# Kernel tuning notes

Measured on AMD Instinct MI355X. Metric: run time of the kernel, lower is better.

Reference implementation:

```python
import jax, jax.numpy as jnp
import numpy as np

N_EMBD = 1024
N_HEAD = 16
HEAD_DIM = N_EMBD // N_HEAD
SCALE = 1.0 / np.sqrt(HEAD_DIM).astype(np.float32)


def setup_inputs() -> dict:
    key = jax.random.key(0)
    ks = jax.random.split(key, 9)
    B, T = 2, 2048
    std = 1.0 / np.sqrt(N_EMBD).astype(np.float32)
    x = jax.random.normal(ks[0], (B, T, N_EMBD), dtype=jnp.float32)
    Wq = jax.random.normal(ks[1], (N_EMBD, N_EMBD), dtype=jnp.float32) * std
    Wk = jax.random.normal(ks[2], (N_EMBD, N_EMBD), dtype=jnp.float32) * std
    Wv = jax.random.normal(ks[3], (N_EMBD, N_EMBD), dtype=jnp.float32) * std
    Wo = jax.random.normal(ks[4], (N_EMBD, N_EMBD), dtype=jnp.float32) * std
    bq = jax.random.normal(ks[5], (N_EMBD,), dtype=jnp.float32) * 0.01
    bk = jax.random.normal(ks[6], (N_EMBD,), dtype=jnp.float32) * 0.01
    bv = jax.random.normal(ks[7], (N_EMBD,), dtype=jnp.float32) * 0.01
    bo = jax.random.normal(ks[8], (N_EMBD,), dtype=jnp.float32) * 0.01
    return {"x": x, "Wq": Wq, "bq": bq, "Wk": Wk, "bk": bk,
            "Wv": Wv, "bv": bv, "Wo": Wo, "bo": bo}


def reference(x, Wq, bq, Wk, bk, Wv, bv, Wo, bo):
    B, T, C = x.shape
    # project and split heads: (B, H, T, D)
    def heads(y):
        return y.reshape(B, T, N_HEAD, HEAD_DIM).transpose(0, 2, 1, 3)
    q = heads(x @ Wq.T + bq)
    k = heads(x @ Wk.T + bk)
    v = heads(x @ Wv.T + bv)
    # materialized causal attention (matches the torch module's math)
    att = jnp.einsum("bhqd,bhkd->bhqk", q, k) * SCALE
    causal = jnp.tril(jnp.ones((T, T), dtype=bool))
    att = jnp.where(causal, att, -jnp.inf)
    att = jax.nn.softmax(att, axis=-1)
    out = jnp.einsum("bhqk,bhkd->bhqd", att, v)
    out = out.transpose(0, 2, 1, 3).reshape(B, T, C)
    return out @ Wo.T + bo
```

## Files before the change

kernel.cpp:

```cpp
#include <hip/hip_runtime.h>
#include <stdint.h>

typedef unsigned short u16;
typedef __attribute__((ext_vector_type(8))) short short8;
typedef __attribute__((ext_vector_type(4))) float f32x4;
typedef __attribute__((ext_vector_type(16))) float f32x16;

__device__ __forceinline__ u16 f2bf(float f) {
  union { float f; unsigned int u; } c; c.f = f;
  return (u16)((c.u + 0x7FFFu + ((c.u >> 16) & 1u)) >> 16);
}

__device__ __forceinline__ float bf2f(u16 v) {
  union { unsigned int u; float f; } c; c.u = ((unsigned int)v) << 16;
  return c.f;
}

__device__ __forceinline__ f32x4 mfma16(short8 a, short8 b, f32x4 c) {
  return __builtin_amdgcn_mfma_f32_16x16x32_bf16(a, b, c, 0, 0, 0);
}

__device__ __forceinline__ f32x16 mfma32(short8 a, short8 b, f32x16 c) {
  return __builtin_amdgcn_mfma_f32_32x32x16_bf16(a, b, c, 0, 0, 0);
}

__device__ __forceinline__ void gl_lds16(const u16* g, u16* l) {
  __builtin_amdgcn_global_load_lds((const __attribute__((address_space(1))) void*)g,
                                   (__attribute__((address_space(3))) void*)l, 16, 0, 0);
}

__global__ __launch_bounds__(256) void cast_all(
    const float* __restrict__ x, const float* __restrict__ wq, const float* __restrict__ wk,
    const float* __restrict__ wv, const float* __restrict__ wo,
    u16* __restrict__ xb, u16* __restrict__ wqb, u16* __restrict__ wkb,
    u16* __restrict__ wvb, u16* __restrict__ wob) {
  int b = blockIdx.x;
  const float* src; u16* dst; int i;
  if (b < 4096)      { src = x;  dst = xb;  i = b * 256 + threadIdx.x; }
  else if (b < 5120) { src = wq; dst = wqb; i = (b - 4096) * 256 + threadIdx.x; }
  else if (b < 6144) { src = wk; dst = wkb; i = (b - 5120) * 256 + threadIdx.x; }
  else if (b < 7168) { src = wv; dst = wvb; i = (b - 6144) * 256 + threadIdx.x; }
  else               { src = wo; dst = wob; i = (b - 7168) * 256 + threadIdx.x; }
  float4 v = ((const float4*)src)[i];
  ushort4 o;
  o.x = f2bf(v.x); o.y = f2bf(v.y); o.z = f2bf(v.z); o.w = f2bf(v.w);
  ((ushort4*)dst)[i] = o;
}

__global__ __launch_bounds__(256) void qkv_gemm(
    const u16* __restrict__ xb, const u16* __restrict__ wqb, const u16* __restrict__ wkb,
    const u16* __restrict__ wvb, const float* __restrict__ bq, const float* __restrict__ bk,
    const float* __restrict__ bv, u16* __restrict__ Qb, u16* __restrict__ Kb,
    u16* __restrict__ VTb) {
  __shared__ __align__(16) u16 As[128 * 64];
  __shared__ __align__(16) u16 Bs[128 * 64];
  const int id = blockIdx.x;
  const int s = id >> 3;
  const int mblk = (id & 7) + ((s & 3) << 3);
  const int z = (s >> 2) % 3;
  const int nblk = s / 12;
  const u16* __restrict__ W = (z == 0) ? wqb : (z == 1) ? wkb : wvb;
  const float* __restrict__ bias = (z == 0) ? bq : (z == 1) ? bk : bv;
  const int m0 = mblk * 128, n0 = nblk * 128;
  const int tid = threadIdx.x, lane = tid & 63, wave = tid >> 6;
  const int wr = (wave >> 1) * 64, wc = (wave & 1) * 64;
  const int fr = lane & 15, fg = lane >> 4;
  const int lrow = lane >> 3;
  const int lcol = (((lane & 7) ^ (lrow & 7)) * 8);

  const u16* ga = xb + (size_t)(m0 + wave * 32 + lrow) * 1024 + lcol;
  const u16* gb = W  + (size_t)(n0 + wave * 32 + lrow) * 1024 + lcol;
  u16* la = As + wave * 2048;
  u16* lb = Bs + wave * 2048;

  f32x4 acc[4][4] = {};

  for (int k0 = 0; k0 < 1024; k0 += 64) {
#pragma unroll
    for (int i = 0; i < 4; ++i) {
      gl_lds16(ga + k0 + (size_t)(8 * i) * 1024, la + i * 512);
      gl_lds16(gb + k0 + (size_t)(8 * i) * 1024, lb + i * 512);
    }
    __syncthreads();
#pragma unroll
    for (int kk = 0; kk < 2; ++kk) {
      short8 a[4], b[4];
#pragma unroll
      for (int i = 0; i < 4; ++i)
        a[i] = *(const short8*)(As + (wr + i * 16 + fr) * 64 +
                                (((kk * 4 + fg) ^ (fr & 7)) * 8));
#pragma unroll
      for (int i = 0; i < 4; ++i)
        b[i] = *(const short8*)(Bs + (wc + i * 16 + fr) * 64 +
                                (((kk * 4 + fg) ^ (fr & 7)) * 8));
#pragma unroll
      for (int i = 0; i < 4; ++i)
#pragma unroll
        for (int j = 0; j < 4; ++j) acc[i][j] = mfma16(a[i], b[j], acc[i][j]);
    }
    __syncthreads();
  }

  const float qsc = (z == 0) ? (0.125f * 1.44269504088896f) : 1.0f;
#pragma unroll
  for (int j = 0; j < 4; ++j) {
    const int col = n0 + wc + j * 16 + fr;
    const float bcol = bias[col];
    const int h = col >> 6, d = col & 63;
#pragma unroll
    for (int i = 0; i < 4; ++i) {
#pragma unroll
      for (int r = 0; r < 4; ++r) {
        const int m = m0 + wr + i * 16 + fg * 4 + r;
        const int bi = m >> 11, t = m & 2047;
        const u16 o = f2bf((acc[i][j][r] + bcol) * qsc);
        const size_t bse = (size_t)(bi * 16 + h) << 17;
        if (z == 0)      Qb[bse + (size_t)t * 64 + d] = o;
        else if (z == 1) Kb[bse + (size_t)t * 64 + d] = o;
        else             VTb[bse + (size_t)d * 2048 + t] = o;
      }
    }
  }
}

__global__ __launch_bounds__(256, 2) void attn_kernel(
    const u16* __restrict__ Qb, const u16* __restrict__ Kb, const u16* __restrict__ VTb,
    u16* __restrict__ aOb) {
  __shared__ __align__(16) char smem[49152];
  __shared__ float Mll[4][2][64];
  u16* Ow = (u16*)smem;
  const int id = blockIdx.x;
  const int xcd = id & 7, wbl = id >> 3;
  const int cu = wbl & 31, rr = wbl >> 5;
  const int g = cu >> 2;
  const int bh = xcd + ((cu & 3) << 3);
  const int j = (rr == 0) ? 31 - g : (rr == 1) ? 16 + g : (rr == 2) ? 15 - g : g;
  const int tid = threadIdx.x, lane = tid & 63, wave = tid >> 6;
  const int l31 = lane & 31, hi = lane >> 5;
  const size_t base = (size_t)bh << 17;
  const int bi = bh >> 4, h = bh & 15;
  const int q0 = j * 64;

  u16* kb0 = (u16*)(smem + wave * 12288);
  u16* kb1 = (u16*)(smem + wave * 12288 + 4096);
  u16* vb  = (u16*)(smem + wave * 12288 + 8192);

  short8 qf[2][4];
  {
    const u16* qp = Qb + base + (size_t)(q0 + l31) * 64 + hi * 8;
#pragma unroll
    for (int mi = 0; mi < 2; ++mi)
#pragma unroll
      for (int st = 0; st < 4; ++st)
        qf[mi][st] = *(const short8*)(qp + mi * 32 * 64 + st * 16);
  }

  f32x16 oacc[2][2] = {};
  float lrun[2] = {0.f, 0.f};

  auto stageK = [&](int t0, u16* kb) {
    const u16* kp = Kb + base + (size_t)(t0 + (lane >> 3)) * 64 +
                    (((lane & 7) ^ ((lane >> 3) & 7)) * 8);
#pragma unroll
    for (int i = 0; i < 4; ++i) gl_lds16(kp + (size_t)(8 * i) * 64, kb + i * 512);
  };
  auto stageV = [&](int t0) {
    const u16* vp = VTb + base + (size_t)(lane >> 2) * 2048 + t0 +
                    (((lane & 3) ^ ((lane >> 2) & 3)) * 8);
#pragma unroll
    for (int i = 0; i < 4; ++i) gl_lds16(vp + (size_t)(16 * i) * 2048, vb + i * 512);
  };

  const int tmax = 2 * j + 1;
  if (wave <= tmax) {
    int buf = 0;
    stageK(wave * 32, kb0);
    stageV(wave * 32);
    for (int tu = wave; tu <= tmax; tu += 4) {
      const int t0 = tu * 32;
      const bool more = (tu + 4 <= tmax);
      if (more) {
        stageK((tu + 4) * 32, buf ? kb0 : kb1);
        asm volatile("s_waitcnt vmcnt(4)" ::: "memory");
      } else {
        asm volatile("s_waitcnt vmcnt(0)" ::: "memory");
      }
      __builtin_amdgcn_sched_barrier(0);
      const char* kb = (const char*)(buf ? kb1 : kb0);

      short8 kf[4];
#pragma unroll
      for (int st = 0; st < 4; ++st)
        kf[st] = *(const short8*)(kb + l31 * 128 + (((st * 2 + hi) ^ (l31 & 7)) << 4));
      short8 vf[2][2];
#pragma unroll
      for (int nb = 0; nb < 2; ++nb)
#pragma unroll
        for (int ks = 0; ks < 2; ++ks)
          vf[nb][ks] = *(const short8*)((const char*)vb + (nb * 32 + l31) * 64 +
                                        (((ks * 2 + hi) ^ (l31 & 3)) << 4));

#pragma unroll
      for (int mi = 0; mi < 2; ++mi) {
        f32x16 s = {};
        __builtin_amdgcn_s_setprio(1);
        s = mfma32(kf[0], qf[mi][0], s);
        s = mfma32(kf[1], qf[mi][1], s);
        s = mfma32(kf[2], qf[mi][2], s);
        s = mfma32(kf[3], qf[mi][3], s);
        __builtin_amdgcn_s_setprio(0);

        if (t0 + 31 > q0 + mi * 32) {
          const int qv = q0 + mi * 32 + l31;
#pragma unroll
          for (int r = 0; r < 16; ++r) {
            const int tl = t0 + (r & 3) + ((r >> 2) << 3) + hi * 4;
            if (tl > qv) s[r] = -1e30f;
          }
        }

        float rs = 0.f;
#pragma unroll
        for (int r = 0; r < 16; ++r) {
          const float pv = exp2f(s[r]);
          s[r] = pv;
          rs += pv;
        }
        lrun[mi] += rs;

        uint32_t w0, w1, w2, w3, w4, w5, w6, w7;
        asm("v_cvt_pk_bf16_f32 %0, %1, %2" : "=v"(w0) : "v"(s[0]),  "v"(s[1]));
        asm("v_cvt_pk_bf16_f32 %0, %1, %2" : "=v"(w1) : "v"(s[2]),  "v"(s[3]));
        asm("v_cvt_pk_bf16_f32 %0, %1, %2" : "=v"(w2) : "v"(s[4]),  "v"(s[5]));
        asm("v_cvt_pk_bf16_f32 %0, %1, %2" : "=v"(w3) : "v"(s[6]),  "v"(s[7]));
        asm("v_cvt_pk_bf16_f32 %0, %1, %2" : "=v"(w4) : "v"(s[8]),  "v"(s[9]));
        asm("v_cvt_pk_bf16_f32 %0, %1, %2" : "=v"(w5) : "v"(s[10]), "v"(s[11]));
        asm("v_cvt_pk_bf16_f32 %0, %1, %2" : "=v"(w6) : "v"(s[12]), "v"(s[13]));
        asm("v_cvt_pk_bf16_f32 %0, %1, %2" : "=v"(w7) : "v"(s[14]), "v"(s[15]));
        asm("v_permlane32_swap_b32 %0, %1" : "+v"(w0), "+v"(w2));
        asm("v_permlane32_swap_b32 %0, %1" : "+v"(w1), "+v"(w3));
        asm("v_permlane32_swap_b32 %0, %1" : "+v"(w4), "+v"(w6));
        asm("v_permlane32_swap_b32 %0, %1" : "+v"(w5), "+v"(w7));
        short8 pa0, pa1;
        {
          uint32_t* p0 = (uint32_t*)&pa0;
          p0[0] = w0; p0[1] = w1; p0[2] = w2; p0[3] = w3;
          uint32_t* p1 = (uint32_t*)&pa1;
          p1[0] = w4; p1[1] = w5; p1[2] = w6; p1[3] = w7;
        }

        __builtin_amdgcn_s_setprio(1);
        oacc[mi][0] = mfma32(pa0, vf[0][0], oacc[mi][0]);
        oacc[mi][0] = mfma32(pa1, vf[0][1], oacc[mi][0]);
        oacc[mi][1] = mfma32(pa0, vf[1][0], oacc[mi][1]);
        oacc[mi][1] = mfma32(pa1, vf[1][1], oacc[mi][1]);
        __builtin_amdgcn_s_setprio(0);
      }

      if (more) {
        asm volatile("s_waitcnt lgkmcnt(0)" ::: "memory");
        __builtin_amdgcn_sched_barrier(0);
        stageV((tu + 4) * 32);
      }
      buf ^= 1;
    }
  }

  __syncthreads();
#pragma unroll
  for (int mi = 0; mi < 2; ++mi) Mll[wave][hi][mi * 32 + l31] = lrun[mi];
#pragma unroll
  for (int mi = 0; mi < 2; ++mi)
#pragma unroll
    for (int nb = 0; nb < 2; ++nb)
#pragma unroll
      for (int r = 0; r < 16; ++r) {
        const int q = mi * 32 + (r & 3) + ((r >> 2) << 3) + hi * 4;
        Ow[(wave * 64 + q) * 72 + nb * 32 + l31] = f2bf(oacc[mi][nb][r]);
      }
  __syncthreads();

  const int rq = tid >> 2, c0 = (tid & 3) * 16;
  float lt = 0.f;
#pragma unroll
  for (int w = 0; w < 4; ++w)
#pragma unroll
    for (int gg = 0; gg < 2; ++gg) lt += Mll[w][gg][rq];
  const float inv = __builtin_amdgcn_rcpf(lt);
  float o[16] = {};
#pragma unroll
  for (int w = 0; w < 4; ++w) {
    const u16* orow = &Ow[(w * 64 + rq) * 72 + c0];
    short8 a = *(const short8*)orow;
    short8 b = *(const short8*)(orow + 8);
#pragma unroll
    for (int i = 0; i < 8; ++i) {
      o[i]     += bf2f((u16)a[i]);
      o[8 + i] += bf2f((u16)b[i]);
    }
  }
  short8 r0, r1;
#pragma unroll
  for (int i = 0; i < 8; ++i) {
    r0[i] = (short)f2bf(o[i] * inv);
    r1[i] = (short)f2bf(o[8 + i] * inv);
  }
  u16* op = aOb + ((size_t)bi * 2048 + q0 + rq) * 1024 + h * 64 + c0;
  *(short8*)op = r0;
  *(short8*)(op + 8) = r1;
}

__global__ __launch_bounds__(256) void out_gemm(
    const u16* __restrict__ Ab, const u16* __restrict__ Wb, const float* __restrict__ bo,
    float* __restrict__ out) {
  __shared__ __align__(16) u16 As[128 * 64];
  __shared__ __align__(16) u16 Bs[128 * 64];
  const int id = blockIdx.x;
  const int s = id >> 3;
  const int m0 = ((id & 7) + ((s & 3) << 3)) * 128;
  const int n0 = (s >> 2) * 128;
  const int tid = threadIdx.x, lane = tid & 63, wave = tid >> 6;
  const int wr = (wave >> 1) * 64, wc = (wave & 1) * 64;
  const int fr = lane & 15, fg = lane >> 4;
  const int lrow = lane >> 3;
  const int lcol = (((lane & 7) ^ (lrow & 7)) * 8);

  const u16* ga = Ab + (size_t)(m0 + wave * 32 + lrow) * 1024 + lcol;
  const u16* gb = Wb + (size_t)(n0 + wave * 32 + lrow) * 1024 + lcol;
  u16* la = As + wave * 2048;
  u16* lb = Bs + wave * 2048;

  f32x4 acc[4][4] = {};

  for (int k0 = 0; k0 < 1024; k0 += 64) {
#pragma unroll
    for (int i = 0; i < 4; ++i) {
      gl_lds16(ga + k0 + (size_t)(8 * i) * 1024, la + i * 512);
      gl_lds16(gb + k0 + (size_t)(8 * i) * 1024, lb + i * 512);
    }
    __syncthreads();
#pragma unroll
    for (int kk = 0; kk < 2; ++kk) {
      short8 a[4], b[4];
#pragma unroll
      for (int i = 0; i < 4; ++i)
        a[i] = *(const short8*)(As + (wr + i * 16 + fr) * 64 +
                                (((kk * 4 + fg) ^ (fr & 7)) * 8));
#pragma unroll
      for (int i = 0; i < 4; ++i)
        b[i] = *(const short8*)(Bs + (wc + i * 16 + fr) * 64 +
                                (((kk * 4 + fg) ^ (fr & 7)) * 8));
#pragma unroll
      for (int i = 0; i < 4; ++i)
#pragma unroll
        for (int j = 0; j < 4; ++j) acc[i][j] = mfma16(a[i], b[j], acc[i][j]);
    }
    __syncthreads();
  }

#pragma unroll
  for (int j = 0; j < 4; ++j) {
    const int col = n0 + wc + j * 16 + fr;
    const float bcol = bo[col];
#pragma unroll
    for (int i = 0; i < 4; ++i)
#pragma unroll
      for (int r = 0; r < 4; ++r) {
        const int m = m0 + wr + i * 16 + fg * 4 + r;
        out[(size_t)m * 1024 + col] = acc[i][j][r] + bcol;
      }
  }
}

extern "C" void kernel_launch(void* const* d_in, const int* in_sizes, int n_in,
                              void* d_out, int out_size, void* d_ws, size_t ws_size,
                              hipStream_t stream) {
  (void)in_sizes; (void)n_in; (void)out_size; (void)ws_size;
  const float* x  = (const float*)d_in[0];
  const float* Wq = (const float*)d_in[1];
  const float* bq = (const float*)d_in[2];
  const float* Wk = (const float*)d_in[3];
  const float* bk = (const float*)d_in[4];
  const float* Wv = (const float*)d_in[5];
  const float* bv = (const float*)d_in[6];
  const float* Wo = (const float*)d_in[7];
  const float* bo = (const float*)d_in[8];
  float* out = (float*)d_out;
  char* ws = (char*)d_ws;

  const size_t MB = 1024 * 1024;
  u16* xb  = (u16*)(ws);
  u16* wqb = (u16*)(ws + 8 * MB);
  u16* wkb = (u16*)(ws + 10 * MB);
  u16* wvb = (u16*)(ws + 12 * MB);
  u16* wob = (u16*)(ws + 14 * MB);
  u16* Qb  = (u16*)(ws + 16 * MB);
  u16* Kb  = (u16*)(ws + 24 * MB);
  u16* VTb = (u16*)(ws + 32 * MB);
  u16* aOb = (u16*)(ws + 40 * MB);

  cast_all<<<8192, 256, 0, stream>>>(x, Wq, Wk, Wv, Wo, xb, wqb, wkb, wvb, wob);
  qkv_gemm<<<768, 256, 0, stream>>>(xb, wqb, wkb, wvb, bq, bk, bv, Qb, Kb, VTb);
  attn_kernel<<<1024, 256, 0, stream>>>(Qb, Kb, VTb, aOb);
  out_gemm<<<256, 256, 0, stream>>>(aOb, wob, bo, out);
}
```

Baseline: 122.0 us.

## Double-buffer LDS tiles in QKV and output GEMMs to overlap loads with MFMA

Both projection GEMMs now use two LDS buffers per operand and issue the global-to-LDS loads for the next K tile before computing on the current one, with one barrier per iteration instead of two. This is meant to hide global memory latency behind MFMA work. MFMA sections are also wrapped in s_setprio raises so waves doing math are favoured by the scheduler. LDS use per block doubles to 64KB, which can reduce occupancy.

```diff
diff --git a/kernel.cpp b/kernel.cpp
--- a/kernel.cpp
+++ b/kernel.cpp
@@ -52,8 +52,8 @@
     const u16* __restrict__ wvb, const float* __restrict__ bq, const float* __restrict__ bk,
     const float* __restrict__ bv, u16* __restrict__ Qb, u16* __restrict__ Kb,
     u16* __restrict__ VTb) {
-  __shared__ __align__(16) u16 As[128 * 64];
-  __shared__ __align__(16) u16 Bs[128 * 64];
+  __shared__ __align__(16) u16 As[2][128 * 64];
+  __shared__ __align__(16) u16 Bs[2][128 * 64];
   const int id = blockIdx.x;
   const int s = id >> 3;
   const int mblk = (id & 7) + ((s & 3) << 3);
@@ -70,35 +70,51 @@
 
   const u16* ga = xb + (size_t)(m0 + wave * 32 + lrow) * 1024 + lcol;
   const u16* gb = W  + (size_t)(n0 + wave * 32 + lrow) * 1024 + lcol;
-  u16* la = As + wave * 2048;
-  u16* lb = Bs + wave * 2048;
-
-  f32x4 acc[4][4] = {};
-
-  for (int k0 = 0; k0 < 1024; k0 += 64) {
+
+  auto stage = [&](int k0, int b) {
+    u16* la = As[b] + wave * 2048;
+    u16* lb = Bs[b] + wave * 2048;
 #pragma unroll
     for (int i = 0; i < 4; ++i) {
       gl_lds16(ga + k0 + (size_t)(8 * i) * 1024, la + i * 512);
       gl_lds16(gb + k0 + (size_t)(8 * i) * 1024, lb + i * 512);
     }
-    __syncthreads();
+  };
+
+  f32x4 acc[4][4] = {};
+
+  stage(0, 0);
+  asm volatile("s_waitcnt vmcnt(0)" ::: "memory");
+  __builtin_amdgcn_s_barrier();
+  __builtin_amdgcn_sched_barrier(0);
+
+  for (int t = 0; t < 16; ++t) {
+    const int cur = t & 1;
+    if (t < 15) stage((t + 1) * 64, cur ^ 1);
+    __builtin_amdgcn_sched_barrier(0);
+    const u16* Ac = As[cur];
+    const u16* Bc = Bs[cur];
 #pragma unroll
     for (int kk = 0; kk < 2; ++kk) {
       short8 a[4], b[4];
 #pragma unroll
       for (int i = 0; i < 4; ++i)
-        a[i] = *(const short8*)(As + (wr + i * 16 + fr) * 64 +
+        a[i] = *(const short8*)(Ac + (wr + i * 16 + fr) * 64 +
                                 (((kk * 4 + fg) ^ (fr & 7)) * 8));
 #pragma unroll
       for (int i = 0; i < 4; ++i)
-        b[i] = *(const short8*)(Bs + (wc + i * 16 + fr) * 64 +
+        b[i] = *(const short8*)(Bc + (wc + i * 16 + fr) * 64 +
                                 (((kk * 4 + fg) ^ (fr & 7)) * 8));
+      __builtin_amdgcn_s_setprio(1);
 #pragma unroll
       for (int i = 0; i < 4; ++i)
 #pragma unroll
         for (int j = 0; j < 4; ++j) acc[i][j] = mfma16(a[i], b[j], acc[i][j]);
-    }
-    __syncthreads();
+      __builtin_amdgcn_s_setprio(0);
+    }
+    asm volatile("s_waitcnt vmcnt(0)" ::: "memory");
+    __builtin_amdgcn_s_barrier();
+    __builtin_amdgcn_sched_barrier(0);
   }
 
   const float qsc = (z == 0) ? (0.125f * 1.44269504088896f) : 1.0f;
@@ -313,8 +329,8 @@
 __global__ __launch_bounds__(256) void out_gemm(
     const u16* __restrict__ Ab, const u16* __restrict__ Wb, const float* __restrict__ bo,
     float* __restrict__ out) {
-  __shared__ __align__(16) u16 As[128 * 64];
-  __shared__ __align__(16) u16 Bs[128 * 64];
+  __shared__ __align__(16) u16 As[2][128 * 64];
+  __shared__ __align__(16) u16 Bs[2][128 * 64];
   const int id = blockIdx.x;
   const int s = id >> 3;
   const int m0 = ((id & 7) + ((s & 3) << 3)) * 128;
@@ -327,35 +343,51 @@
 
   const u16* ga = Ab + (size_t)(m0 + wave * 32 + lrow) * 1024 + lcol;
   const u16* gb = Wb + (size_t)(n0 + wave * 32 + lrow) * 1024 + lcol;
-  u16* la = As + wave * 2048;
-  u16* lb = Bs + wave * 2048;
-
-  f32x4 acc[4][4] = {};
-
-  for (int k0 = 0; k0 < 1024; k0 += 64) {
+
+  auto stage = [&](int k0, int b) {
+    u16* la = As[b] + wave * 2048;
+    u16* lb = Bs[b] + wave * 2048;
 #pragma unroll
     for (int i = 0; i < 4; ++i) {
       gl_lds16(ga + k0 + (size_t)(8 * i) * 1024, la + i * 512);
       gl_lds16(gb + k0 + (size_t)(8 * i) * 1024, lb + i * 512);
     }
-    __syncthreads();
+  };
+
+  f32x4 acc[4][4] = {};
+
+  stage(0, 0);
+  asm volatile("s_waitcnt vmcnt(0)" ::: "memory");
+  __builtin_amdgcn_s_barrier();
+  __builtin_amdgcn_sched_barrier(0);
+
+  for (int t = 0; t < 16; ++t) {
+    const int cur = t & 1;
+    if (t < 15) stage((t + 1) * 64, cur ^ 1);
+    __builtin_amdgcn_sched_barrier(0);
+    const u16* Ac = As[cur];
+    const u16* Bc = Bs[cur];
 #pragma unroll
     for (int kk = 0; kk < 2; ++kk) {
       short8 a[4], b[4];
 #pragma unroll
       for (int i = 0; i < 4; ++i)
-        a[i] = *(const short8*)(As + (wr + i * 16 + fr) * 64 +
+        a[i] = *(const short8*)(Ac + (wr + i * 16 + fr) * 64 +
                                 (((kk * 4 + fg) ^ (fr & 7)) * 8));
 #pragma unroll
       for (int i = 0; i < 4; ++i)
-        b[i] = *(const short8*)(Bs + (wc + i * 16 + fr) * 64 +
+        b[i] = *(const short8*)(Bc + (wc + i * 16 + fr) * 64 +
                                 (((kk * 4 + fg) ^ (fr & 7)) * 8));
+      __builtin_amdgcn_s_setprio(1);
 #pragma unroll
       for (int i = 0; i < 4; ++i)
 #pragma unroll
         for (int j = 0; j < 4; ++j) acc[i][j] = mfma16(a[i], b[j], acc[i][j]);
-    }
-    __syncthreads();
+      __builtin_amdgcn_s_setprio(0);
+    }
+    asm volatile("s_waitcnt vmcnt(0)" ::: "memory");
+    __builtin_amdgcn_s_barrier();
+    __builtin_amdgcn_sched_barrier(0);
   }
 
 #pragma unroll
```

Result: no change. 123.8 us (+1.5%).
